# Kernel tuning notes

Hardware: AMD Instinct MI355X
Metric: run time of the kernel (lower is better)

The kernel has to match this reference:

```python
import jax, jax.numpy as jnp
from jax import lax
import numpy as np

N_TOTAL = 262144
NUM_SAMPLE = 1024
KNN_K = 16
NUM_CLASSES = 13
HIDDEN = 128
EPS = 1e-8


def _sqdist(a, b):
    # (Na,3),(Nb,3) -> (Na,Nb) squared euclidean; same argmin as torch.cdist
    return (jnp.sum(a * a, axis=1)[:, None]
            + jnp.sum(b * b, axis=1)[None, :]
            - 2.0 * a @ b.T)


def _farthest_point_sample(xyz, n_samples):
    # sequential FPS starting from index 0 (deterministic start)
    n = xyz.shape[0]

    def step(carry, _):
        min_d2, last = carry
        d2 = jnp.sum((xyz - xyz[last]) ** 2, axis=-1)
        min_d2 = jnp.minimum(min_d2, d2)
        nxt = jnp.argmax(min_d2).astype(jnp.int32)
        return (min_d2, nxt), nxt

    init = (jnp.full((n,), 1e10, dtype=xyz.dtype), jnp.int32(0))
    _, idxs = lax.scan(step, init, None, length=n_samples - 1)
    return jnp.concatenate([jnp.zeros((1,), jnp.int32), idxs])


def _compute_normals(pts, k):
    # PCA normal per point from its k nearest neighbors (self excluded)
    d2 = _sqdist(pts, pts)                      # (S,S), S=1024 -> small
    _, nbr_idx = lax.top_k(-d2, k + 1)
    nbr = pts[nbr_idx[:, 1:]]                   # (S,k,3)
    centered = nbr - jnp.mean(nbr, axis=1, keepdims=True)
    cov = jnp.einsum('ski,skj->sij', centered, centered) / (k - 1)
    _, eigvecs = jnp.linalg.eigh(cov)           # ascending eigenvalues
    normal = eigvecs[..., 0]                    # smallest-eigval eigenvector
    return normal / (jnp.linalg.norm(normal, axis=-1, keepdims=True) + EPS)


def _forward(gaussian_positions, gaussian_colors, W1, b1, W2, b2, W3, b3):
    sample_idx = _farthest_point_sample(gaussian_positions, NUM_SAMPLE)
    dxyz = gaussian_positions[sample_idx]       # (S,3)
    drgb = gaussian_colors[sample_idx]          # (S,3)
    dnrm = _compute_normals(dxyz, KNN_K)        # (S,3)
    feats = jnp.concatenate([dxyz, drgb, dnrm], axis=1)  # (S,9)

    # pointwise segmentation network (stand-in for PointNet++ get_model)
    h = jax.nn.relu(feats @ W1 + b1)
    h = jax.nn.relu(h @ W2 + b2)
    pred = h @ W3 + b3                          # (S, num_classes)

    feat_down = jax.nn.softmax(pred, axis=1)
    lbl_down = jnp.argmax(pred, axis=1)

    # 1-NN label propagation: streaming-min candidate (memory-bound)
    d2_full = _sqdist(gaussian_positions, dxyz)  # (N, S) ~ 1 GB
    nearest = jnp.argmin(d2_full, axis=1)
    return feat_down[nearest], lbl_down[nearest]


def setup_inputs() -> dict:
    key = jax.random.key(0)
    ks = jax.random.split(key, 8)
    pos = jax.random.normal(ks[0], (N_TOTAL, 3), jnp.float32)
    col = jax.random.uniform(ks[1], (N_TOTAL, 3), jnp.float32)
    W1 = jax.random.normal(ks[2], (9, HIDDEN), jnp.float32) / np.sqrt(9.0)
    b1 = jnp.zeros((HIDDEN,), jnp.float32)
    W2 = jax.random.normal(ks[3], (HIDDEN, HIDDEN), jnp.float32) / np.sqrt(HIDDEN)
    b2 = jnp.zeros((HIDDEN,), jnp.float32)
    W3 = jax.random.normal(ks[4], (HIDDEN, NUM_CLASSES), jnp.float32) / np.sqrt(HIDDEN)
    b3 = jnp.zeros((NUM_CLASSES,), jnp.float32)
    return {"gaussian_positions": pos, "gaussian_colors": col,
            "W1": W1, "b1": b1, "W2": W2, "b2": b2, "W3": W3, "b3": b3}


def reference(gaussian_positions, gaussian_colors, W1, b1, W2, b2, W3, b3):
    return _forward(gaussian_positions, gaussian_colors, W1, b1, W2, b2, W3, b3)
```

## Files before the change

### kernel.cpp

```cpp
#include <hip/hip_runtime.h>
#include <math.h>

#define N_TOTAL    262144
#define NUM_SAMPLE 1024
#define FPS_BLOCKS 64
#define FPS_THREADS 256
#define FPS_PPT (N_TOTAL / (FPS_BLOCKS * FPS_THREADS))
#define M_WAVE 8
#define POOL (FPS_BLOCKS * 4 * M_WAVE)
#define ENT_PER_T (POOL / FPS_THREADS)
#define ACT 512
#define SEL_CAP 1023

__device__ __forceinline__ float addrn(float a, float b) { return __fadd_rn(a, b); }
__device__ __forceinline__ float subrn(float a, float b) { return __fsub_rn(a, b); }
__device__ __forceinline__ float mulrn(float a, float b) { return __fmul_rn(a, b); }

__device__ __forceinline__ float d2rn(float ax, float ay, float az,
                                      float bx, float by, float bz) {
  float dx = subrn(ax, bx), dy = subrn(ay, by), dz = subrn(az, bz);
  return addrn(addrn(mulrn(dx, dx), mulrn(dy, dy)), mulrn(dz, dz));
}

__device__ __forceinline__ bool lex_gt(float m1, unsigned i1, float m2, unsigned i2) {
  return (m1 > m2) || (m1 == m2 && i1 > i2);
}
__device__ __forceinline__ bool lex_ge(float m1, unsigned i1, float m2, unsigned i2) {
  return (m1 > m2) || (m1 == m2 && i1 >= i2);
}

template <int CTRL>
__device__ __forceinline__ int dpp_i(int x) {
  return __builtin_amdgcn_update_dpp(x, x, CTRL, 0xF, 0xF, false);
}
__device__ __forceinline__ float wave_fmax_bcast(float v) {
  v = fmaxf(v, __int_as_float(dpp_i<0x111>(__float_as_int(v))));
  v = fmaxf(v, __int_as_float(dpp_i<0x112>(__float_as_int(v))));
  v = fmaxf(v, __int_as_float(dpp_i<0x114>(__float_as_int(v))));
  v = fmaxf(v, __int_as_float(dpp_i<0x118>(__float_as_int(v))));
  v = fmaxf(v, __int_as_float(dpp_i<0x142>(__float_as_int(v))));
  v = fmaxf(v, __int_as_float(dpp_i<0x143>(__float_as_int(v))));
  return __int_as_float(__builtin_amdgcn_readlane(__float_as_int(v), 63));
}
__device__ __forceinline__ unsigned wave_umax_bcast(unsigned v) {
  unsigned o;
  o = (unsigned)dpp_i<0x111>((int)v); v = (o > v) ? o : v;
  o = (unsigned)dpp_i<0x112>((int)v); v = (o > v) ? o : v;
  o = (unsigned)dpp_i<0x114>((int)v); v = (o > v) ? o : v;
  o = (unsigned)dpp_i<0x118>((int)v); v = (o > v) ? o : v;
  o = (unsigned)dpp_i<0x142>((int)v); v = (o > v) ? o : v;
  o = (unsigned)dpp_i<0x143>((int)v); v = (o > v) ? o : v;
  return (unsigned)__builtin_amdgcn_readlane((int)v, 63);
}

__device__ __forceinline__ float slapy2f(float x, float y) {
  float xa = fabsf(x), ya = fabsf(y);
  float w = fmaxf(xa, ya), z = fminf(xa, ya);
  if (z == 0.f) return w;
  float t = z / w;
  return w * __fsqrt_rn(1.f + t * t);
}

__device__ __forceinline__ void slartgf(float f, float g, float& c, float& s, float& r) {
  if (g == 0.f) { c = 1.f; s = 0.f; r = f; }
  else if (f == 0.f) { c = 0.f; s = (g > 0.f) ? 1.f : -1.f; r = fabsf(g); }
  else {
    float d = __fsqrt_rn(f * f + g * g);
    c = fabsf(f) / d;
    r = (f >= 0.f) ? d : -d;
    s = g / r;
  }
}

__device__ void slaev2f(float a, float b, float c0, float& rt1, float& rt2,
                        float& cs1, float& sn1) {
  float sm = a + c0, df = a - c0;
  float adf = fabsf(df), tb = b + b, ab = fabsf(tb);
  float acmx, acmn;
  if (fabsf(a) > fabsf(c0)) { acmx = a; acmn = c0; } else { acmx = c0; acmn = a; }
  float rt;
  if (adf > ab)      { float t = ab / adf; rt = adf * __fsqrt_rn(1.f + t * t); }
  else if (adf < ab) { float t = adf / ab; rt = ab * __fsqrt_rn(1.f + t * t); }
  else               { rt = ab * __fsqrt_rn(2.f); }
  int sgn1;
  if (sm < 0.f)      { rt1 = 0.5f * (sm - rt); sgn1 = -1; rt2 = (acmx / rt1) * acmn - (b / rt1) * b; }
  else if (sm > 0.f) { rt1 = 0.5f * (sm + rt); sgn1 = 1;  rt2 = (acmx / rt1) * acmn - (b / rt1) * b; }
  else               { rt1 = 0.5f * rt; rt2 = -0.5f * rt; sgn1 = 1; }
  float cs; int sgn2;
  if (df >= 0.f) { cs = df + rt; sgn2 = 1; } else { cs = df - rt; sgn2 = -1; }
  float acs = fabsf(cs);
  if (acs > ab) {
    float ct = -tb / cs;
    sn1 = 1.f / __fsqrt_rn(1.f + ct * ct);
    cs1 = ct * sn1;
  } else {
    if (ab == 0.f) { cs1 = 1.f; sn1 = 0.f; }
    else { float tn = -cs / tb; cs1 = 1.f / __fsqrt_rn(1.f + tn * tn); sn1 = tn * cs1; }
  }
  if (sgn1 == sgn2) { float tn = cs1; cs1 = -sn1; sn1 = tn; }
}

#define D_(i) d[(i)-1]
#define E_(i) e[(i)-1]

__device__ void ssteqr3(float d[3], float e[2], float Z[3][3]) {
  const float eps    = 5.9604645e-08f;
  const float eps2   = 3.5527137e-15f;
  const float safmin = 1.17549435e-38f;
  const float ssfmax = 3.0744573e+18f;
  const float ssfmin = 3.0517578e-05f;
  const int n = 3;
  int jtot = 0, nmaxit = 90;
  int l1 = 1;

  while (true) {
    if (l1 > n) break;
    if (l1 > 1) E_(l1 - 1) = 0.f;
    int m = n;
    for (int mm = l1; mm <= n - 1; ++mm) {
      float tst = fabsf(E_(mm));
      if (tst == 0.f) { m = mm; break; }
      if (tst <= (__fsqrt_rn(fabsf(D_(mm))) * __fsqrt_rn(fabsf(D_(mm + 1)))) * eps) {
        E_(mm) = 0.f; m = mm; break;
      }
    }
    int l = l1, lsv = l, lend = m, lendsv = m;
    l1 = m + 1;
    if (lend == l) continue;

    float anorm = fabsf(D_(lend));
    for (int i2 = l; i2 <= lend - 1; ++i2) {
      anorm = fmaxf(anorm, fabsf(D_(i2)));
      anorm = fmaxf(anorm, fabsf(E_(i2)));
    }
    int iscale = 0;
    if (anorm == 0.f) continue;
    if (anorm > ssfmax) {
      iscale = 1; float mul = ssfmax / anorm;
      for (int i2 = l; i2 <= lend; ++i2) D_(i2) *= mul;
      for (int i2 = l; i2 <= lend - 1; ++i2) E_(i2) *= mul;
    } else if (anorm < ssfmin) {
      iscale = 2; float mul = ssfmin / anorm;
      for (int i2 = l; i2 <= lend; ++i2) D_(i2) *= mul;
      for (int i2 = l; i2 <= lend - 1; ++i2) E_(i2) *= mul;
    }

    if (fabsf(D_(lend)) < fabsf(D_(l))) { int t = l; l = lend; lend = t; }

    if (lend > l) {
      while (true) {
        int m2 = lend;
        if (l != lend) {
          for (int mm = l; mm <= lend - 1; ++mm) {
            float tst = fabsf(E_(mm)); tst = tst * tst;
            if (tst <= (eps2 * fabsf(D_(mm))) * fabsf(D_(mm + 1)) + safmin) { m2 = mm; break; }
          }
        }
        if (m2 < lend) E_(m2) = 0.f;
        float p = D_(l);
        if (m2 == l) { D_(l) = p; l = l + 1; if (l <= lend) continue; break; }
        if (m2 == l + 1) {
          float rt1, rt2, cc, ss;
          slaev2f(D_(l), E_(l), D_(l + 1), rt1, rt2, cc, ss);
          for (int i2 = 0; i2 < 3; ++i2) {
            float tmp = Z[i2][l];
            Z[i2][l]     = cc * tmp - ss * Z[i2][l - 1];
            Z[i2][l - 1] = ss * tmp + cc * Z[i2][l - 1];
          }
          D_(l) = rt1; D_(l + 1) = rt2; E_(l) = 0.f;
          l = l + 2; if (l <= lend) continue; break;
        }
        if (jtot == nmaxit) break;
        ++jtot;
        float g = (D_(l + 1) - p) / (2.f * E_(l));
        float r = slapy2f(g, 1.f);
        float sgn_rg = (g >= 0.f) ? r : -r;
        g = D_(m2) - p + E_(l) / (g + sgn_rg);
        float s = 1.f, c = 1.f;
        p = 0.f;
        float csv[2], ssv[2];
        for (int i2 = m2 - 1; i2 >= l; --i2) {
          float f = s * E_(i2);
          float b = c * E_(i2);
          slartgf(g, f, c, s, r);
          if (i2 != m2 - 1) E_(i2 + 1) = r;
          g = D_(i2 + 1) - p;
          r = (D_(i2) - g) * s + 2.f * c * b;
          p = s * r;
          D_(i2 + 1) = g + p;
          g = c * r - b;
          csv[i2 - l] = c; ssv[i2 - l] = -s;
        }
        for (int j = m2 - 1; j >= l; --j) {
          float ct = csv[j - l], st = ssv[j - l];
          for (int i2 = 0; i2 < 3; ++i2) {
            float tmp = Z[i2][j];
            Z[i2][j]     = ct * tmp - st * Z[i2][j - 1];
            Z[i2][j - 1] = st * tmp + ct * Z[i2][j - 1];
          }
        }
        D_(l) = D_(l) - p;
        E_(l) = g;
      }
    } else {
      while (true) {
        int m2 = lend;
        if (l != lend) {
          for (int mm = l; mm >= lend + 1; --mm) {
            float tst = fabsf(E_(mm - 1)); tst = tst * tst;
            if (tst <= (eps2 * fabsf(D_(mm))) * fabsf(D_(mm - 1)) + safmin) { m2 = mm; break; }
          }
        }
        if (m2 > lend) E_(m2 - 1) = 0.f;
        float p = D_(l);
        if (m2 == l) { D_(l) = p; l = l - 1; if (l >= lend) continue; break; }
        if (m2 == l - 1) {
          float rt1, rt2, cc, ss;
          slaev2f(D_(l - 1), E_(l - 1), D_(l), rt1, rt2, cc, ss);
          for (int i2 = 0; i2 < 3; ++i2) {
            float tmp = Z[i2][l - 1];
            Z[i2][l - 1] = cc * tmp - ss * Z[i2][l - 2];
            Z[i2][l - 2] = ss * tmp + cc * Z[i2][l - 2];
          }
          D_(l - 1) = rt1; D_(l) = rt2; E_(l - 1) = 0.f;
          l = l - 2; if (l >= lend) continue; break;
        }
        if (jtot == nmaxit) break;
        ++jtot;
        float g = (D_(l - 1) - p) / (2.f * E_(l - 1));
        float r = slapy2f(g, 1.f);
        float sgn_rg = (g >= 0.f) ? r : -r;
        g = D_(m2) - p + E_(l - 1) / (g + sgn_rg);
        float s = 1.f, c = 1.f;
        p = 0.f;
        float csv[2], ssv[2];
        for (int i2 = m2; i2 <= l - 1; ++i2) {
          float f = s * E_(i2);
          float b = c * E_(i2);
          slartgf(g, f, c, s, r);
          if (i2 != m2) E_(i2 - 1) = r;
          g = D_(i2) - p;
          r = (D_(i2 + 1) - g) * s + 2.f * c * b;
          p = s * r;
          D_(i2) = g + p;
          g = c * r - b;
          csv[i2 - m2] = c; ssv[i2 - m2] = s;
        }
        for (int j = m2; j <= l - 1; ++j) {
          float ct = csv[j - m2], st = ssv[j - m2];
          for (int i2 = 0; i2 < 3; ++i2) {
            float tmp = Z[i2][j];
            Z[i2][j]     = ct * tmp - st * Z[i2][j - 1];
            Z[i2][j - 1] = st * tmp + ct * Z[i2][j - 1];
          }
        }
        D_(l) = D_(l) - p;
        E_(l - 1) = g;
      }
    }
    if (iscale == 1) {
      float mul = anorm / ssfmax;
      for (int i2 = lsv; i2 <= lendsv; ++i2) D_(i2) *= mul;
      for (int i2 = lsv; i2 <= lendsv - 1; ++i2) E_(i2) *= mul;
    } else if (iscale == 2) {
      float mul = anorm / ssfmin;
      for (int i2 = lsv; i2 <= lendsv; ++i2) D_(i2) *= mul;
      for (int i2 = lsv; i2 <= lendsv - 1; ++i2) E_(i2) *= mul;
    }
  }
  for (int ii = 2; ii <= n; ++ii) {
    int i2 = ii - 1, k = i2;
    float p = D_(i2);
    for (int j = ii; j <= n; ++j) if (D_(j) < p) { k = j; p = D_(j); }
    if (k != i2) {
      D_(k) = D_(i2); D_(i2) = p;
      for (int rr = 0; rr < 3; ++rr) {
        float t = Z[rr][i2 - 1]; Z[rr][i2 - 1] = Z[rr][k - 1]; Z[rr][k - 1] = t;
      }
    }
  }
}

__device__ void eigh3_smallest(float a00, float a10, float a20, float a11, float a21, float a22,
                               float& nx, float& ny, float& nz) {
  float d[3], e[2];
  float Z[3][3] = {{1.f,0.f,0.f},{0.f,1.f,0.f},{0.f,0.f,1.f}};
  float tau, v2;
  {
    float alpha = a10, x = a20;
    float xnorm = fabsf(x);
    if (xnorm == 0.f) {
      tau = 0.f; v2 = 0.f;
      d[0] = a00; d[1] = a11; d[2] = a22;
      e[0] = alpha; e[1] = a21;
    } else {
      float beta = -copysignf(slapy2f(alpha, x), alpha);
      tau = (beta - alpha) / beta;
      v2 = x / (alpha - beta);
      float w0 = (tau * a11) + tau * (a21 * v2);
      float w1 = (tau * a21) + (tau * v2) * a22;
      float ac = (-0.5f * tau) * (w0 + w1 * v2);
      w0 = w0 + ac;
      w1 = w1 + ac * v2;
      d[0] = a00;
      d[1] = (a11 - w0) - w0;
      d[2] = (a22 - v2 * w1) - w1 * v2;
      e[0] = beta;
      e[1] = (a21 - v2 * w0) - w1;
    }
  }
  ssteqr3(d, e, Z);
  if (tau != 0.f) {
    for (int c = 0; c < 3; ++c) {
      float w = Z[1][c] + Z[2][c] * v2;
      float temp = (-tau) * w;
      Z[1][c] = Z[1][c] + temp;
      Z[2][c] = Z[2][c] + v2 * temp;
    }
  }
  nx = Z[0][0]; ny = Z[1][0]; nz = Z[2][0];
}

__global__ void k0_init(unsigned long long* cand, int* sample_idx) {
  int t = blockIdx.x * blockDim.x + threadIdx.x;
  if (t < 2 * POOL) cand[t] = 0ull;
  if (t == 0) sample_idx[0] = 0;
}

__global__ __launch_bounds__(FPS_THREADS) void k1_fps(
    const float* __restrict__ pos,
    unsigned long long* __restrict__ cand,
    int* __restrict__ sample_idx) {
  __shared__ float sel_x[SEL_CAP], sel_y[SEL_CAP], sel_z[SEL_CAP];
  __shared__ float tred_md[4];
  __shared__ unsigned tred_idf[4];
  __shared__ float t2red_md[4];
  __shared__ unsigned t2red_idf[4];
  __shared__ float act_md[ACT], act_x[ACT], act_y[ACT], act_z[ACT];
  __shared__ unsigned act_idf[ACT];
  __shared__ float thr3_md[FPS_THREADS];
  __shared__ unsigned thr3_idf[FPS_THREADS];
  __shared__ int sh_flag, sh_pc;

  const int tidx = threadIdx.x;
  const int lane = tidx & 63, wv = tidx >> 6;
  const int gtid = blockIdx.x * FPS_THREADS + tidx;

  float px[FPS_PPT], py[FPS_PPT], pz[FPS_PPT], md[FPS_PPT];
#pragma unroll
  for (int k = 0; k < FPS_PPT; ++k) {
    int p = gtid + k * (FPS_BLOCKS * FPS_THREADS);
    px[k] = pos[3 * p]; py[k] = pos[3 * p + 1]; pz[k] = pos[3 * p + 2];
    md[k] = 1e10f;
  }
  const unsigned idf0 = 0x3FFFFFu - (unsigned)gtid;
  if (tidx == 0) { sel_x[0] = pos[0]; sel_y[0] = pos[1]; sel_z[0] = pos[2]; }
  __syncthreads();
  int sel_cnt = 1, total = 0, bt = 0;
  while (total < NUM_SAMPLE - 1) {
    ++bt;
    for (int s = 0; s < sel_cnt; ++s) {
      float lx = sel_x[s], ly = sel_y[s], lz = sel_z[s];
#pragma unroll
      for (int k = 0; k < FPS_PPT; ++k)
        md[k] = fminf(md[k], d2rn(px[k], py[k], pz[k], lx, ly, lz));
    }
    const unsigned tag = (unsigned)bt & 1023u;
    unsigned long long* setbase = cand + (size_t)(bt & 1) * POOL;
    {
      float wmd[FPS_PPT];
#pragma unroll
      for (int k = 0; k < FPS_PPT; ++k) wmd[k] = md[k];
      unsigned long long mypub = 0ull;
      for (int r = 0; r < M_WAVE; ++r) {
        float bm = wmd[0]; unsigned bidf = idf0;
#pragma unroll
        for (int k = 1; k < FPS_PPT; ++k) {
          unsigned idfk = idf0 - ((unsigned)k << 14);
          if (wmd[k] > bm || (wmd[k] == bm && idfk > bidf)) { bm = wmd[k]; bidf = idfk; }
        }
        float wmx = wave_fmax_bcast(bm);
        unsigned tb = (bm == wmx) ? bidf : 0u;
        unsigned widf = wave_umax_bcast(tb);
        if (lane == r)
          mypub = ((unsigned long long)__float_as_uint(wmx) << 32) |
                  ((unsigned long long)widf << 10);
#pragma unroll
        for (int k = 0; k < FPS_PPT; ++k) {
          unsigned idfk = idf0 - ((unsigned)k << 14);
          if (wmd[k] == wmx && idfk == widf) wmd[k] = -1.f;
        }
      }
      if (lane < M_WAVE)
        __hip_atomic_store(setbase + blockIdx.x * (4 * M_WAVE) + wv * M_WAVE + lane,
                           mypub | tag, __ATOMIC_RELAXED, __HIP_MEMORY_SCOPE_AGENT);
    }
    const int base_w = tidx * ENT_PER_T;
    float cmd[ENT_PER_T]; unsigned cidf[ENT_PER_T];
    float cx[ENT_PER_T], cy[ENT_PER_T], cz[ENT_PER_T];
    {
      unsigned done = 0;
      while (done != 0xFFu) {
#pragma unroll
        for (int j = 0; j < ENT_PER_T; ++j) {
          if (!((done >> j) & 1u)) {
            unsigned long long v = __hip_atomic_load(setbase + base_w + j,
                                                     __ATOMIC_RELAXED, __HIP_MEMORY_SCOPE_AGENT);
            if ((unsigned)(v & 1023ull) == tag) {
              done |= 1u << j;
              cmd[j] = __uint_as_float((unsigned)(v >> 32));
              cidf[j] = (unsigned)((v >> 10) & 0x3FFFFFull);
              int gidx = 0x3FFFFF - (int)cidf[j];
              cx[j] = pos[3 * gidx]; cy[j] = pos[3 * gidx + 1]; cz[j] = pos[3 * gidx + 2];
            }
          }
        }
        if (done != 0xFFu) __builtin_amdgcn_s_sleep(1);
      }
    }
    {
      float t7 = cmd[ENT_PER_T - 1]; unsigned t7i = cidf[ENT_PER_T - 1];
      float w7 = wave_fmax_bcast(t7);
      unsigned tb7 = (t7 == w7) ? t7i : 0u;
      unsigned w7i = wave_umax_bcast(tb7);
      if (lane == 0) { tred_md[wv] = w7; tred_idf[wv] = w7i; }
      float t2 = cmd[2]; unsigned t2i = cidf[2];
      float w2 = wave_fmax_bcast(t2);
      unsigned tb2 = (t2 == w2) ? t2i : 0u;
      unsigned w2i = wave_umax_bcast(tb2);
      if (lane == 0) { t2red_md[wv] = w2; t2red_idf[wv] = w2i; }
      int e = 2 * tidx;
      act_md[e] = cmd[0]; act_idf[e] = cidf[0];
      act_x[e] = cx[0]; act_y[e] = cy[0]; act_z[e] = cz[0];
      act_md[e + 1] = cmd[1]; act_idf[e + 1] = cidf[1];
      act_x[e + 1] = cx[1]; act_y[e + 1] = cy[1]; act_z[e + 1] = cz[1];
    }
    __syncthreads();
    float Tmd = tred_md[0]; unsigned Tidf = tred_idf[0];
    float T2m = t2red_md[0]; unsigned T2i = t2red_idf[0];
#pragma unroll
    for (int w = 1; w < 4; ++w) {
      if (lex_gt(tred_md[w], tred_idf[w], Tmd, Tidf)) { Tmd = tred_md[w]; Tidf = tred_idf[w]; }
      if (lex_gt(t2red_md[w], t2red_idf[w], T2m, T2i)) { T2m = t2red_md[w]; T2i = t2red_idf[w]; }
    }
    const int room = (NUM_SAMPLE - 1) - total;
    float q_md[8], q_x[8], q_y[8], q_z[8];
    unsigned q_idf[8];
    if (tidx < 64) {
#pragma unroll
      for (int r = 0; r < 8; ++r) {
        int e2 = lane + 64 * r;
        q_md[r] = act_md[e2]; q_idf[r] = act_idf[e2];
        q_x[r] = act_x[e2]; q_y[r] = act_y[e2]; q_z[r] = act_z[e2];
      }
    }
    int picks = 0, myq = 0, pc = 0;
    for (;;) {
      if (tidx < 64) {
        int ev = 0;
        for (;;) {
          float bm = q_md[0]; unsigned bidf = q_idf[0];
          float bx = q_x[0], by = q_y[0], bz = q_z[0];
#pragma unroll
          for (int j = 1; j < 8; ++j) {
            bool g = (q_md[j] > bm) || (q_md[j] == bm && q_idf[j] > bidf);
            if (g) { bm = q_md[j]; bidf = q_idf[j]; bx = q_x[j]; by = q_y[j]; bz = q_z[j]; }
          }
          float wmx = wave_fmax_bcast(bm);
          unsigned long long ball = __ballot(bm == wmx);
          unsigned widf; int owner;
          if (__builtin_popcountll(ball) == 1) {
            owner = __builtin_ctzll(ball);
            widf = (unsigned)__builtin_amdgcn_readlane((int)bidf, owner);
          } else {
            unsigned tb = (bm == wmx) ? bidf : 0u;
            widf = wave_umax_bcast(tb);
            owner = __builtin_ctzll(__ballot(bm == wmx && bidf == widf));
          }
          if (picks >= room) { ev = 0; break; }
          if (!lex_ge(wmx, widf, T2m, T2i)) { ev = 1; break; }
          if (!lex_ge(wmx, widf, Tmd, Tidf)) { ev = 0; break; }
          float X = __int_as_float(__builtin_amdgcn_readlane(__float_as_int(bx), owner));
          float Y = __int_as_float(__builtin_amdgcn_readlane(__float_as_int(by), owner));
          float Z = __int_as_float(__builtin_amdgcn_readlane(__float_as_int(bz), owner));
          if (lane == 0) {
            sel_x[picks] = X; sel_y[picks] = Y; sel_z[picks] = Z;
            if (blockIdx.x == 0) sample_idx[1 + total + picks] = 0x3FFFFF - (int)widf;
          }
#pragma unroll
          for (int j = 0; j < 8; ++j)
            q_md[j] = fminf(q_md[j], d2rn(q_x[j], q_y[j], q_z[j], X, Y, Z));
          ++picks;
        }
        if (lane == 0) { sh_flag = ev; sh_pc = picks; }
      }
      __syncthreads();
      int ev = sh_flag; pc = sh_pc;
      if (ev == 0) break;
      for (int q = myq; q < pc; ++q) {
        float lx = sel_x[q], ly = sel_y[q], lz = sel_z[q];
#pragma unroll
        for (int j = 0; j < ENT_PER_T; ++j)
          cmd[j] = fminf(cmd[j], d2rn(cx[j], cy[j], cz[j], lx, ly, lz));
      }
      myq = pc;
      {
        float m1 = -1.f, m2 = -1.f, m3 = -1.f;
        unsigned i1 = 0u, i2v = 0u, i3v = 0u;
        float x1 = 0.f, y1 = 0.f, z1 = 0.f, x2 = 0.f, y2 = 0.f, z2 = 0.f;
#pragma unroll
        for (int j = 0; j < ENT_PER_T; ++j) {
          float m = cmd[j]; unsigned ii = cidf[j];
          float xx = cx[j], yy = cy[j], zz = cz[j];
          bool g1 = lex_gt(m, ii, m1, i1);
          bool g2 = lex_gt(m, ii, m2, i2v);
          bool g3 = lex_gt(m, ii, m3, i3v);
          float nm3 = g2 ? m2 : (g3 ? m : m3); unsigned ni3 = g2 ? i2v : (g3 ? ii : i3v);
          float nm2 = g1 ? m1 : (g2 ? m : m2); unsigned ni2 = g1 ? i1 : (g2 ? ii : i2v);
          float nx2 = g1 ? x1 : (g2 ? xx : x2);
          float ny2 = g1 ? y1 : (g2 ? yy : y2);
          float nz2 = g1 ? z1 : (g2 ? zz : z2);
          float nm1 = g1 ? m : m1; unsigned ni1 = g1 ? ii : i1;
          float nx1 = g1 ? xx : x1;
          float ny1 = g1 ? yy : y1;
          float nz1 = g1 ? zz : z1;
          m3 = nm3; i3v = ni3;
          m2 = nm2; i2v = ni2; x2 = nx2; y2 = ny2; z2 = nz2;
          m1 = nm1; i1 = ni1; x1 = nx1; y1 = ny1; z1 = nz1;
        }
        int e = 2 * tidx;
        act_md[e] = m1; act_idf[e] = i1; act_x[e] = x1; act_y[e] = y1; act_z[e] = z1;
        act_md[e + 1] = m2; act_idf[e + 1] = i2v;
        act_x[e + 1] = x2; act_y[e + 1] = y2; act_z[e + 1] = z2;
        thr3_md[tidx] = m3; thr3_idf[tidx] = i3v;
      }
      __syncthreads();
      if (tidx < 64) {
#pragma unroll
        for (int r = 0; r < 8; ++r) {
          int e2 = lane + 64 * r;
          q_md[r] = act_md[e2]; q_idf[r] = act_idf[e2];
          q_x[r] = act_x[e2]; q_y[r] = act_y[e2]; q_z[r] = act_z[e2];
        }
        float rm = thr3_md[lane]; unsigned ri = thr3_idf[lane];
#pragma unroll
        for (int r = 1; r < 4; ++r) {
          float m = thr3_md[lane + 64 * r]; unsigned ii = thr3_idf[lane + 64 * r];
          if (lex_gt(m, ii, rm, ri)) { rm = m; ri = ii; }
        }
        float wm = wave_fmax_bcast(rm);
        unsigned tb = (rm == wm) ? ri : 0u;
        unsigned wi = wave_umax_bcast(tb);
        T2m = wm; T2i = wi;
      }
    }
    sel_cnt = pc;
    total += pc;
  }
}

__global__ __launch_bounds__(256) void k2a_knn(
    const float* __restrict__ pos, const float* __restrict__ col,
    const int* __restrict__ sample_idx,
    float4* __restrict__ sp4g, float* __restrict__ feats9) {
  __shared__ float4 sp[NUM_SAMPLE];
  const int tid = threadIdx.x, lane = tid & 63, wv = tid >> 6;
  for (int i = tid; i < NUM_SAMPLE; i += 256) {
    int idx = sample_idx[i];
    float x = pos[3 * idx], y = pos[3 * idx + 1], z = pos[3 * idx + 2];
    float nrm = addrn(addrn(mulrn(x, x), mulrn(y, y)), mulrn(z, z));
    float4 v = make_float4(x, y, z, nrm);
    sp[i] = v;
    if (blockIdx.x == 0) sp4g[i] = v;
  }
  __syncthreads();
  for (int it = 0; it < 4; ++it) {
    const int r = blockIdx.x * 16 + wv * 4 + it;
    float4 pr = sp[r];
    unsigned long long kk[16];
#pragma unroll
    for (int k = 0; k < 16; ++k) {
      int j = lane + 64 * k;
      float4 q = sp[j];
      float dot = fmaf(pr.z, q.z, fmaf(pr.y, q.y, mulrn(pr.x, q.x)));
      float d2 = subrn(addrn(pr.w, q.w), mulrn(2.f, dot));
      unsigned b = __float_as_uint(d2);
      unsigned sbits = (b & 0x80000000u) ? ~b : (b | 0x80000000u);
      kk[k] = ((unsigned long long)sbits << 32) | (unsigned)j;
    }
    int bi[17];
#pragma unroll
    for (int rsel = 0; rsel < 17; ++rsel) {
      unsigned long long best = 0xFFFFFFFFFFFFFFFFull;
#pragma unroll
      for (int k = 0; k < 16; ++k) best = (kk[k] < best) ? kk[k] : best;
#pragma unroll
      for (int mk = 1; mk < 64; mk <<= 1) {
        unsigned long long o = (unsigned long long)__shfl_xor((long long)best, mk, 64);
        best = (o < best) ? o : best;
      }
      int j = (int)(best & 0xFFFFFFFFull);
      bi[rsel] = j;
#pragma unroll
      for (int k = 0; k < 16; ++k)
        if (((j >> 6) == k) && ((j & 63) == lane)) kk[k] = 0xFFFFFFFFFFFFFFFFull;
    }
    float mx = 0.f, my = 0.f, mz = 0.f;
#pragma unroll
    for (int k = 1; k <= 16; ++k) {
      float4 q = sp[bi[k]];
      mx = addrn(mx, q.x); my = addrn(my, q.y); mz = addrn(mz, q.z);
    }
    mx = mulrn(mx, 0.0625f); my = mulrn(my, 0.0625f); mz = mulrn(mz, 0.0625f);
    float c00 = 0.f, c01 = 0.f, c02 = 0.f, c11 = 0.f, c12 = 0.f, c22 = 0.f;
#pragma unroll
    for (int k = 1; k <= 16; ++k) {
      float4 q = sp[bi[k]];
      float dx = subrn(q.x, mx), dy = subrn(q.y, my), dz = subrn(q.z, mz);
      c00 = addrn(c00, mulrn(dx, dx)); c01 = addrn(c01, mulrn(dx, dy));
      c02 = addrn(c02, mulrn(dx, dz)); c11 = addrn(c11, mulrn(dy, dy));
      c12 = addrn(c12, mulrn(dy, dz)); c22 = addrn(c22, mulrn(dz, dz));
    }
    c00 /= 15.f; c01 /= 15.f; c02 /= 15.f; c11 /= 15.f; c12 /= 15.f; c22 /= 15.f;

    float n0, n1, n2;
    eigh3_smallest(c00, c01, c02, c11, c12, c22, n0, n1, n2);
    float nn = __fsqrt_rn(addrn(addrn(mulrn(n0, n0), mulrn(n1, n1)), mulrn(n2, n2)));
    float den = addrn(nn, 1e-8f);
    n0 /= den; n1 /= den; n2 /= den;

    if (lane == 0) {
      int myidx = sample_idx[r];
      float* f = feats9 + r * 9;
      f[0] = pr.x; f[1] = pr.y; f[2] = pr.z;
      f[3] = col[3 * myidx]; f[4] = col[3 * myidx + 1]; f[5] = col[3 * myidx + 2];
      f[6] = n0; f[7] = n1; f[8] = n2;
    }
  }
}

__global__ __launch_bounds__(64) void k2b_mlp(
    const float* __restrict__ W1, const float* __restrict__ b1,
    const float* __restrict__ W2, const float* __restrict__ b2,
    const float* __restrict__ W3, const float* __restrict__ b3,
    const float* __restrict__ feats9,
    float* __restrict__ featd, int* __restrict__ lbl) {
  __shared__ float hbuf[64][129];
  const int tid = threadIdx.x;
  const int r = blockIdx.x * 64 + tid;
  float f9[9];
#pragma unroll
  for (int k = 0; k < 9; ++k) f9[k] = feats9[r * 9 + k];
  for (int jo = 0; jo < 128; ++jo) {
    float acc = 0.f;
#pragma unroll
    for (int k = 0; k < 9; ++k) acc = fmaf(f9[k], W1[k * 128 + jo], acc);
    acc += b1[jo];
    hbuf[tid][jo] = fmaxf(acc, 0.f);
  }
  float pd[13];
#pragma unroll
  for (int c = 0; c < 13; ++c) pd[c] = 0.f;
  for (int io = 0; io < 128; io += 16) {
    float acc[16];
#pragma unroll
    for (int t = 0; t < 16; ++t) acc[t] = 0.f;
    for (int j = 0; j < 128; ++j) {
      float hj = hbuf[tid][j];
#pragma unroll
      for (int t = 0; t < 16; ++t) acc[t] = fmaf(hj, W2[j * 128 + io + t], acc[t]);
    }
#pragma unroll
    for (int t = 0; t < 16; ++t) {
      float h2 = fmaxf(acc[t] + b2[io + t], 0.f);
#pragma unroll
      for (int c = 0; c < 13; ++c) pd[c] = fmaf(h2, W3[(io + t) * 13 + c], pd[c]);
    }
  }
#pragma unroll
  for (int c = 0; c < 13; ++c) pd[c] += b3[c];
  float mmax = pd[0];
#pragma unroll
  for (int c = 1; c < 13; ++c) mmax = fmaxf(mmax, pd[c]);
  float es = 0.f, ev[13];
#pragma unroll
  for (int c = 0; c < 13; ++c) { ev[c] = expf(pd[c] - mmax); es += ev[c]; }
#pragma unroll
  for (int c = 0; c < 13; ++c) featd[r * 13 + c] = ev[c] / es;
  int am = 0; float bv = pd[0];
#pragma unroll
  for (int c = 1; c < 13; ++c) { if (pd[c] > bv) { bv = pd[c]; am = c; } }
  lbl[r] = am;
}

__global__ __launch_bounds__(256) void k3_assign(
    const float* __restrict__ pos,
    const float4* __restrict__ sp4g,
    const float* __restrict__ featd,
    const int* __restrict__ lbl,
    float* __restrict__ out) {
  __shared__ float4 sp[NUM_SAMPLE];
  for (int i = threadIdx.x; i < NUM_SAMPLE; i += 256) sp[i] = sp4g[i];
  __syncthreads();
  int i = blockIdx.x * 256 + threadIdx.x;
  float x = pos[3 * i], y = pos[3 * i + 1], z = pos[3 * i + 2];
  float an = addrn(addrn(mulrn(x, x), mulrn(y, y)), mulrn(z, z));
  float bestd = 3.402823466e+38f; int bestj = 0;
#pragma unroll 4
  for (int j = 0; j < NUM_SAMPLE; ++j) {
    float4 q = sp[j];
    float dot = fmaf(z, q.z, fmaf(y, q.y, mulrn(x, q.x)));
    float d2 = subrn(addrn(an, q.w), mulrn(2.f, dot));
    if (d2 < bestd) { bestd = d2; bestj = j; }
  }
  const float* fr = featd + bestj * 13;
  float* o = out + (size_t)i * 13;
#pragma unroll
  for (int c = 0; c < 13; ++c) o[c] = fr[c];
  out[(size_t)N_TOTAL * 13 + i] = (float)lbl[bestj];
}

extern "C" void kernel_launch(void* const* d_in, const int* in_sizes, int n_in,
                              void* d_out, int out_size, void* d_ws, size_t ws_size,
                              hipStream_t stream) {
  (void)in_sizes; (void)n_in; (void)out_size; (void)ws_size;
  const float* pos = (const float*)d_in[0];
  const float* col = (const float*)d_in[1];
  const float* W1 = (const float*)d_in[2];
  const float* b1 = (const float*)d_in[3];
  const float* W2 = (const float*)d_in[4];
  const float* b2 = (const float*)d_in[5];
  const float* W3 = (const float*)d_in[6];
  const float* b3 = (const float*)d_in[7];
  float* out = (float*)d_out;

  char* w = (char*)d_ws;
  unsigned long long* cand = (unsigned long long*)(w);
  int* sample_idx = (int*)(w + 65536);
  float4* sp4g = (float4*)(w + 73728);
  float* featd = (float*)(w + 90112);
  int* lbl = (int*)(w + 143360);
  float* feats9 = (float*)(w + 147456);

  k0_init<<<16, 256, 0, stream>>>(cand, sample_idx);
  k1_fps<<<FPS_BLOCKS, FPS_THREADS, 0, stream>>>(pos, cand, sample_idx);
  k2a_knn<<<64, 256, 0, stream>>>(pos, col, sample_idx, sp4g, feats9);
  k2b_mlp<<<16, 64, 0, stream>>>(W1, b1, W2, b2, W3, b3, feats9, featd, lbl);
  k3_assign<<<N_TOTAL / 256, 256, 0, stream>>>(pos, sp4g, featd, lbl, out);
}
```

Baseline: 1.827 ms.

## Widen FPS candidate pool to 16 per wave with deeper top-k selection

Each wave now publishes 16 candidate maxima per FPS round instead of 8. The per-thread candidate refinement keeps a top-5 instead of a top-3 list, and the active set grows to 1024 entries. The aim is to accept more farthest points per global exchange round, cutting the number of cross-block synchronisation rounds in the sequential FPS. The selected-point buffer moves to float4 with a software-prefetched next entry, and the threshold reductions are restructured. The cost is more register pressure, more atomic polling and more shared memory per round.

New measurement: 2.583 ms. 41.3% more time.

```diff
diff --git a/kernel.cpp b/kernel.cpp
--- a/kernel.cpp
+++ b/kernel.cpp
@@ -6,10 +6,12 @@
 #define FPS_BLOCKS 64
 #define FPS_THREADS 256
 #define FPS_PPT (N_TOTAL / (FPS_BLOCKS * FPS_THREADS))
-#define M_WAVE 8
+#define M_WAVE 16
 #define POOL (FPS_BLOCKS * 4 * M_WAVE)
 #define ENT_PER_T (POOL / FPS_THREADS)
-#define ACT 512
+#define ACT_PER_T 4
+#define ACT (FPS_THREADS * ACT_PER_T)
+#define QD (ACT / 64)
 #define SEL_CAP 1023
 
 __device__ __forceinline__ float addrn(float a, float b) { return __fadd_rn(a, b); }
@@ -327,23 +329,21 @@
   if (t == 0) sample_idx[0] = 0;
 }
 
-__global__ __launch_bounds__(FPS_THREADS) void k1_fps(
+__global__ __launch_bounds__(FPS_THREADS, 1) void k1_fps(
     const float* __restrict__ pos,
     unsigned long long* __restrict__ cand,
     int* __restrict__ sample_idx) {
-  __shared__ float sel_x[SEL_CAP], sel_y[SEL_CAP], sel_z[SEL_CAP];
-  __shared__ float tred_md[4];
-  __shared__ unsigned tred_idf[4];
-  __shared__ float t2red_md[4];
-  __shared__ unsigned t2red_idf[4];
+  __shared__ float4 sel4[SEL_CAP];
   __shared__ float act_md[ACT], act_x[ACT], act_y[ACT], act_z[ACT];
   __shared__ unsigned act_idf[ACT];
-  __shared__ float thr3_md[FPS_THREADS];
-  __shared__ unsigned thr3_idf[FPS_THREADS];
+  __shared__ float thr5_md[FPS_THREADS];
+  __shared__ unsigned thr5_idf[FPS_THREADS];
+  __shared__ float thrT_md[FPS_THREADS];
+  __shared__ unsigned thrT_idf[FPS_THREADS];
   __shared__ int sh_flag, sh_pc;
 
   const int tidx = threadIdx.x;
-  const int lane = tidx & 63, wv = tidx >> 6;
+  const int lane = tidx & 63;
   const int gtid = blockIdx.x * FPS_THREADS + tidx;
 
   float px[FPS_PPT], py[FPS_PPT], pz[FPS_PPT], md[FPS_PPT];
@@ -354,20 +354,25 @@
     md[k] = 1e10f;
   }
   const unsigned idf0 = 0x3FFFFFu - (unsigned)gtid;
-  if (tidx == 0) { sel_x[0] = pos[0]; sel_y[0] = pos[1]; sel_z[0] = pos[2]; }
+  if (tidx == 0) sel4[0] = make_float4(pos[0], pos[1], pos[2], 0.f);
   __syncthreads();
   int sel_cnt = 1, total = 0, bt = 0;
   while (total < NUM_SAMPLE - 1) {
     ++bt;
-    for (int s = 0; s < sel_cnt; ++s) {
-      float lx = sel_x[s], ly = sel_y[s], lz = sel_z[s];
-#pragma unroll
-      for (int k = 0; k < FPS_PPT; ++k)
-        md[k] = fminf(md[k], d2rn(px[k], py[k], pz[k], lx, ly, lz));
+    {
+      float4 sc = sel4[0];
+      for (int s = 0; s < sel_cnt; ++s) {
+        float4 sn = (s + 1 < sel_cnt) ? sel4[s + 1] : sc;
+#pragma unroll
+        for (int k = 0; k < FPS_PPT; ++k)
+          md[k] = fminf(md[k], d2rn(px[k], py[k], pz[k], sc.x, sc.y, sc.z));
+        sc = sn;
+      }
     }
     const unsigned tag = (unsigned)bt & 1023u;
     unsigned long long* setbase = cand + (size_t)(bt & 1) * POOL;
     {
+      const int wv = tidx >> 6;
       float wmd[FPS_PPT];
 #pragma unroll
       for (int k = 0; k < FPS_PPT; ++k) wmd[k] = md[k];
@@ -400,7 +405,7 @@
     float cx[ENT_PER_T], cy[ENT_PER_T], cz[ENT_PER_T];
     {
       unsigned done = 0;
-      while (done != 0xFFu) {
+      while (done != 0xFFFFu) {
 #pragma unroll
         for (int j = 0; j < ENT_PER_T; ++j) {
           if (!((done >> j) & 1u)) {
@@ -415,44 +420,50 @@
             }
           }
         }
-        if (done != 0xFFu) __builtin_amdgcn_s_sleep(1);
+        if (done != 0xFFFFu) __builtin_amdgcn_s_sleep(1);
       }
     }
     {
-      float t7 = cmd[ENT_PER_T - 1]; unsigned t7i = cidf[ENT_PER_T - 1];
-      float w7 = wave_fmax_bcast(t7);
-      unsigned tb7 = (t7 == w7) ? t7i : 0u;
-      unsigned w7i = wave_umax_bcast(tb7);
-      if (lane == 0) { tred_md[wv] = w7; tred_idf[wv] = w7i; }
-      float t2 = cmd[2]; unsigned t2i = cidf[2];
-      float w2 = wave_fmax_bcast(t2);
-      unsigned tb2 = (t2 == w2) ? t2i : 0u;
-      unsigned w2i = wave_umax_bcast(tb2);
-      if (lane == 0) { t2red_md[wv] = w2; t2red_idf[wv] = w2i; }
-      int e = 2 * tidx;
-      act_md[e] = cmd[0]; act_idf[e] = cidf[0];
-      act_x[e] = cx[0]; act_y[e] = cy[0]; act_z[e] = cz[0];
-      act_md[e + 1] = cmd[1]; act_idf[e + 1] = cidf[1];
-      act_x[e + 1] = cx[1]; act_y[e + 1] = cy[1]; act_z[e + 1] = cz[1];
+      int e = ACT_PER_T * tidx;
+#pragma unroll
+      for (int k = 0; k < ACT_PER_T; ++k) {
+        act_md[e + k] = cmd[k]; act_idf[e + k] = cidf[k];
+        act_x[e + k] = cx[k]; act_y[e + k] = cy[k]; act_z[e + k] = cz[k];
+      }
+      thr5_md[tidx] = cmd[ACT_PER_T]; thr5_idf[tidx] = cidf[ACT_PER_T];
+      thrT_md[tidx] = cmd[ENT_PER_T - 1]; thrT_idf[tidx] = cidf[ENT_PER_T - 1];
     }
     __syncthreads();
-    float Tmd = tred_md[0]; unsigned Tidf = tred_idf[0];
-    float T2m = t2red_md[0]; unsigned T2i = t2red_idf[0];
-#pragma unroll
-    for (int w = 1; w < 4; ++w) {
-      if (lex_gt(tred_md[w], tred_idf[w], Tmd, Tidf)) { Tmd = tred_md[w]; Tidf = tred_idf[w]; }
-      if (lex_gt(t2red_md[w], t2red_idf[w], T2m, T2i)) { T2m = t2red_md[w]; T2i = t2red_idf[w]; }
-    }
     const int room = (NUM_SAMPLE - 1) - total;
-    float q_md[8], q_x[8], q_y[8], q_z[8];
-    unsigned q_idf[8];
+    float q_md[QD], q_x[QD], q_y[QD], q_z[QD];
+    unsigned q_idf[QD];
+    float Tmd = 0.f, T2m = 0.f;
+    unsigned Tidf = 0u, T2i = 0u;
     if (tidx < 64) {
 #pragma unroll
-      for (int r = 0; r < 8; ++r) {
+      for (int r = 0; r < QD; ++r) {
         int e2 = lane + 64 * r;
         q_md[r] = act_md[e2]; q_idf[r] = act_idf[e2];
         q_x[r] = act_x[e2]; q_y[r] = act_y[e2]; q_z[r] = act_z[e2];
       }
+      float rm = thrT_md[lane]; unsigned ri = thrT_idf[lane];
+#pragma unroll
+      for (int r = 1; r < 4; ++r) {
+        float m = thrT_md[lane + 64 * r]; unsigned ii = thrT_idf[lane + 64 * r];
+        if (lex_gt(m, ii, rm, ri)) { rm = m; ri = ii; }
+      }
+      Tmd = wave_fmax_bcast(rm);
+      unsigned tbT = (rm == Tmd) ? ri : 0u;
+      Tidf = wave_umax_bcast(tbT);
+      float rm2 = thr5_md[lane]; unsigned ri2 = thr5_idf[lane];
+#pragma unroll
+      for (int r = 1; r < 4; ++r) {
+        float m = thr5_md[lane + 64 * r]; unsigned ii = thr5_idf[lane + 64 * r];
+        if (lex_gt(m, ii, rm2, ri2)) { rm2 = m; ri2 = ii; }
+      }
+      T2m = wave_fmax_bcast(rm2);
+      unsigned tb2 = (rm2 == T2m) ? ri2 : 0u;
+      T2i = wave_umax_bcast(tb2);
     }
     int picks = 0, myq = 0, pc = 0;
     for (;;) {
@@ -462,7 +473,7 @@
           float bm = q_md[0]; unsigned bidf = q_idf[0];
           float bx = q_x[0], by = q_y[0], bz = q_z[0];
 #pragma unroll
-          for (int j = 1; j < 8; ++j) {
+          for (int j = 1; j < QD; ++j) {
             bool g = (q_md[j] > bm) || (q_md[j] == bm && q_idf[j] > bidf);
             if (g) { bm = q_md[j]; bidf = q_idf[j]; bx = q_x[j]; by = q_y[j]; bz = q_z[j]; }
           }
@@ -484,11 +495,11 @@
           float Y = __int_as_float(__builtin_amdgcn_readlane(__float_as_int(by), owner));
           float Z = __int_as_float(__builtin_amdgcn_readlane(__float_as_int(bz), owner));
           if (lane == 0) {
-            sel_x[picks] = X; sel_y[picks] = Y; sel_z[picks] = Z;
+            sel4[picks] = make_float4(X, Y, Z, 0.f);
             if (blockIdx.x == 0) sample_idx[1 + total + picks] = 0x3FFFFF - (int)widf;
           }
 #pragma unroll
-          for (int j = 0; j < 8; ++j)
+          for (int j = 0; j < QD; ++j)
             q_md[j] = fminf(q_md[j], d2rn(q_x[j], q_y[j], q_z[j], X, Y, Z));
           ++picks;
         }
@@ -497,17 +508,22 @@
       __syncthreads();
       int ev = sh_flag; pc = sh_pc;
       if (ev == 0) break;
-      for (int q = myq; q < pc; ++q) {
-        float lx = sel_x[q], ly = sel_y[q], lz = sel_z[q];
-#pragma unroll
-        for (int j = 0; j < ENT_PER_T; ++j)
-          cmd[j] = fminf(cmd[j], d2rn(cx[j], cy[j], cz[j], lx, ly, lz));
-      }
-      myq = pc;
+      if (myq < pc) {
+        float4 sc = sel4[myq];
+        for (int q = myq; q < pc; ++q) {
+          float4 sn = (q + 1 < pc) ? sel4[q + 1] : sc;
+#pragma unroll
+          for (int j = 0; j < ENT_PER_T; ++j)
+            cmd[j] = fminf(cmd[j], d2rn(cx[j], cy[j], cz[j], sc.x, sc.y, sc.z));
+          sc = sn;
+        }
+        myq = pc;
+      }
       {
-        float m1 = -1.f, m2 = -1.f, m3 = -1.f;
-        unsigned i1 = 0u, i2v = 0u, i3v = 0u;
+        float m1 = -1.f, m2 = -1.f, m3 = -1.f, m4 = -1.f, m5 = -1.f;
+        unsigned i1 = 0u, i2v = 0u, i3v = 0u, i4v = 0u, i5v = 0u;
         float x1 = 0.f, y1 = 0.f, z1 = 0.f, x2 = 0.f, y2 = 0.f, z2 = 0.f;
+        float x3 = 0.f, y3 = 0.f, z3 = 0.f, x4 = 0.f, y4 = 0.f, z4 = 0.f;
 #pragma unroll
         for (int j = 0; j < ENT_PER_T; ++j) {
           float m = cmd[j]; unsigned ii = cidf[j];
@@ -515,37 +531,37 @@
           bool g1 = lex_gt(m, ii, m1, i1);
           bool g2 = lex_gt(m, ii, m2, i2v);
           bool g3 = lex_gt(m, ii, m3, i3v);
-          float nm3 = g2 ? m2 : (g3 ? m : m3); unsigned ni3 = g2 ? i2v : (g3 ? ii : i3v);
-          float nm2 = g1 ? m1 : (g2 ? m : m2); unsigned ni2 = g1 ? i1 : (g2 ? ii : i2v);
-          float nx2 = g1 ? x1 : (g2 ? xx : x2);
-          float ny2 = g1 ? y1 : (g2 ? yy : y2);
-          float nz2 = g1 ? z1 : (g2 ? zz : z2);
-          float nm1 = g1 ? m : m1; unsigned ni1 = g1 ? ii : i1;
-          float nx1 = g1 ? xx : x1;
-          float ny1 = g1 ? yy : y1;
-          float nz1 = g1 ? zz : z1;
-          m3 = nm3; i3v = ni3;
-          m2 = nm2; i2v = ni2; x2 = nx2; y2 = ny2; z2 = nz2;
-          m1 = nm1; i1 = ni1; x1 = nx1; y1 = ny1; z1 = nz1;
-        }
-        int e = 2 * tidx;
-        act_md[e] = m1; act_idf[e] = i1; act_x[e] = x1; act_y[e] = y1; act_z[e] = z1;
-        act_md[e + 1] = m2; act_idf[e + 1] = i2v;
-        act_x[e + 1] = x2; act_y[e + 1] = y2; act_z[e + 1] = z2;
-        thr3_md[tidx] = m3; thr3_idf[tidx] = i3v;
+          bool g4 = lex_gt(m, ii, m4, i4v);
+          bool g5 = lex_gt(m, ii, m5, i5v);
+          m5 = g4 ? m4 : (g5 ? m : m5); i5v = g4 ? i4v : (g5 ? ii : i5v);
+          m4 = g3 ? m3 : (g4 ? m : m4); i4v = g3 ? i3v : (g4 ? ii : i4v);
+          x4 = g3 ? x3 : (g4 ? xx : x4); y4 = g3 ? y3 : (g4 ? yy : y4); z4 = g3 ? z3 : (g4 ? zz : z4);
+          m3 = g2 ? m2 : (g3 ? m : m3); i3v = g2 ? i2v : (g3 ? ii : i3v);
+          x3 = g2 ? x2 : (g3 ? xx : x3); y3 = g2 ? y2 : (g3 ? yy : y3); z3 = g2 ? z2 : (g3 ? zz : z3);
+          m2 = g1 ? m1 : (g2 ? m : m2); i2v = g1 ? i1 : (g2 ? ii : i2v);
+          x2 = g1 ? x1 : (g2 ? xx : x2); y2 = g1 ? y1 : (g2 ? yy : y2); z2 = g1 ? z1 : (g2 ? zz : z2);
+          m1 = g1 ? m : m1; i1 = g1 ? ii : i1;
+          x1 = g1 ? xx : x1; y1 = g1 ? yy : y1; z1 = g1 ? zz : z1;
+        }
+        int e = ACT_PER_T * tidx;
+        act_md[e]     = m1; act_idf[e]     = i1;  act_x[e]     = x1; act_y[e]     = y1; act_z[e]     = z1;
+        act_md[e + 1] = m2; act_idf[e + 1] = i2v; act_x[e + 1] = x2; act_y[e + 1] = y2; act_z[e + 1] = z2;
+        act_md[e + 2] = m3; act_idf[e + 2] = i3v; act_x[e + 2] = x3; act_y[e + 2] = y3; act_z[e + 2] = z3;
+        act_md[e + 3] = m4; act_idf[e + 3] = i4v; act_x[e + 3] = x4; act_y[e + 3] = y4; act_z[e + 3] = z4;
+        thr5_md[tidx] = m5; thr5_idf[tidx] = i5v;
       }
       __syncthreads();
       if (tidx < 64) {
 #pragma unroll
-        for (int r = 0; r < 8; ++r) {
+        for (int r = 0; r < QD; ++r) {
           int e2 = lane + 64 * r;
           q_md[r] = act_md[e2]; q_idf[r] = act_idf[e2];
           q_x[r] = act_x[e2]; q_y[r] = act_y[e2]; q_z[r] = act_z[e2];
         }
-        float rm = thr3_md[lane]; unsigned ri = thr3_idf[lane];
+        float rm = thr5_md[lane]; unsigned ri = thr5_idf[lane];
 #pragma unroll
         for (int r = 1; r < 4; ++r) {
-          float m = thr3_md[lane + 64 * r]; unsigned ii = thr3_idf[lane + 64 * r];
+          float m = thr5_md[lane + 64 * r]; unsigned ii = thr5_idf[lane + 64 * r];
           if (lex_gt(m, ii, rm, ri)) { rm = m; ri = ii; }
         }
         float wm = wave_fmax_bcast(rm);
@@ -742,7 +758,7 @@
   int* lbl = (int*)(w + 143360);
   float* feats9 = (float*)(w + 147456);
 
-  k0_init<<<16, 256, 0, stream>>>(cand, sample_idx);
+  k0_init<<<32, 256, 0, stream>>>(cand, sample_idx);
   k1_fps<<<FPS_BLOCKS, FPS_THREADS, 0, stream>>>(pos, cand, sample_idx);
   k2a_knn<<<64, 256, 0, stream>>>(pos, col, sample_idx, sp4g, feats9);
   k2b_mlp<<<16, 64, 0, stream>>>(W1, b1, W2, b2, W3, b3, feats9, featd, lbl);
```
